# Kernel optimization log

Hardware: AMD Instinct MI355X
Metric: run time of the kernel (lower is better)

Reference implementation:

```python
import jax, jax.numpy as jnp
import numpy as np

B, H, E = 16384, 2048, 64
BASE_CF, MIN_CF, MAX_CF = 1.25, 1.0, 2.0


def setup_inputs() -> dict:
    key = jax.random.key(0)
    ks = jax.random.split(key, 4)
    return {
        "hidden_states": jax.random.normal(ks[0], (B, H), jnp.float32),
        "router_w": (jax.random.normal(ks[1], (E, H), jnp.float32) * 0.02),
        "cap_w1": (jax.random.normal(ks[2], (H // 4, H), jnp.float32) * 0.02),
        "cap_b1": jnp.zeros((H // 4,), jnp.float32),
        "cap_w2": (jax.random.normal(ks[3], (E, H // 4), jnp.float32) * 0.02),
        "cap_b2": jnp.zeros((E,), jnp.float32),
    }


def reference(hidden_states, router_w, cap_w1, cap_b1, cap_w2, cap_b2):
    n_tok = hidden_states.shape[0]
    n_exp = router_w.shape[0]

    # router
    router_logits = hidden_states @ router_w.T                      # [B, E]
    router_probs = jax.nn.softmax(router_logits, axis=-1)           # [B, E]

    # dynamic capacity prediction from mean token
    mean_h = hidden_states.mean(axis=0)                             # [H]
    h = jax.nn.relu(mean_h @ cap_w1.T + cap_b1)                     # [H/4]
    cap_logits = h @ cap_w2.T + cap_b2                              # [E]
    cap_weights = jax.nn.softmax(cap_logits)
    cap_factors = jnp.clip(BASE_CF + (cap_weights - 0.5) * (MAX_CF - MIN_CF), MIN_CF, MAX_CF)
    # int() truncation in torch == floor for positive values
    capacity = jnp.floor(n_tok * cap_factors / n_exp).astype(jnp.int32)  # [E]

    # per-expert descending rank of each token's prob (double argsort)
    ranks = jnp.argsort(jnp.argsort(-router_probs, axis=0), axis=0)      # [B, E]
    in_topk = ranks < capacity[None, :]                                  # [B, E]

    e_idx = jnp.arange(n_exp, dtype=jnp.int32)
    sel = jnp.max(jnp.where(in_topk, e_idx[None, :], -1), axis=1)        # [B]
    selections = jnp.where(sel >= 0, sel, 0).astype(jnp.int32)
    w = jnp.take_along_axis(router_probs, selections[:, None], axis=1)[:, 0]
    weights = jnp.where(sel >= 0, w, 0.0)

    entropy = -(router_probs * jnp.log(router_probs + 1e-8)).sum(axis=-1).mean()
    return router_logits, selections[:, None], weights[:, None], entropy
```

## Files before the change

### kernel.cpp

```cpp
#include <hip/hip_runtime.h>
#include <cstdint>

#define TOK 16384
#define HD 2048
#define NE 64
#define HQ 512
#define KC 64
#define NCH (HD / KC)
#define ESCALE 1073741824.0f

__global__ __launch_bounds__(256, 2) void k_router(const float* __restrict__ hid,
                                                   const float* __restrict__ rw,
                                                   float* __restrict__ logits,
                                                   float* __restrict__ csP) {
  __shared__ __align__(16) float As[2][32][KC];
  __shared__ __align__(16) float Bs[2][64][KC];
  __shared__ float red[2][4][64];
  const int tid = threadIdx.x;
  const int lane = tid & 63;
  const int w = tid >> 6;
  const int tm = lane >> 3, tn = lane & 7;
  const int tsub = w >> 1, ehalf = w & 1;
  const int t0 = blockIdx.x * 32;
  const int arow = tid >> 3;
  const int apr = tid & 7;
  const int brow = tid >> 2;
  const int bpr = (tid & 3) * 2;
  const float* hap = hid + (size_t)(t0 + arow) * HD + apr * 8;
  const float* bap = rw + (size_t)brow * HD + (tid & 3) * 16;
  const int aswz = arow & 7;
  const int bswz = (brow >> 2) & 7;
  const int aoff = ((apr ^ aswz) << 3);
  const int boff0 = (((bpr + 0) ^ bswz) << 3);
  const int boff1 = (((bpr + 1) ^ bswz) << 3);

  float4 va0 = *(const float4*)(hap);
  float4 va1 = *(const float4*)(hap + 4);
  float4 vb0 = *(const float4*)(bap);
  float4 vb1 = *(const float4*)(bap + 4);
  float4 vb2 = *(const float4*)(bap + 8);
  float4 vb3 = *(const float4*)(bap + 12);

  float acc[2][4];
#pragma unroll
  for (int i = 0; i < 2; ++i)
#pragma unroll
    for (int j = 0; j < 4; ++j) acc[i][j] = 0.f;

  const int rA0 = tsub * 16 + tm;
  const int rB0 = ehalf * 32 + tn * 4;

  for (int c = 0; c < NCH; ++c) {
    const int cur = c & 1;
    *(float4*)&As[cur][arow][aoff] = va0;
    *(float4*)&As[cur][arow][aoff + 4] = va1;
    *(float4*)&Bs[cur][brow][boff0] = vb0;
    *(float4*)&Bs[cur][brow][boff0 + 4] = vb1;
    *(float4*)&Bs[cur][brow][boff1] = vb2;
    *(float4*)&Bs[cur][brow][boff1 + 4] = vb3;
    if (c + 1 < NCH) {
      va0 = *(const float4*)(hap + (c + 1) * KC);
      va1 = *(const float4*)(hap + (c + 1) * KC + 4);
      vb0 = *(const float4*)(bap + (c + 1) * KC);
      vb1 = *(const float4*)(bap + (c + 1) * KC + 4);
      vb2 = *(const float4*)(bap + (c + 1) * KC + 8);
      vb3 = *(const float4*)(bap + (c + 1) * KC + 12);
    }
    __syncthreads();
    if (c > 0 && tid < 64) {
      const int pb = cur ^ 1;
      float v = red[pb][0][tid] + red[pb][1][tid] + red[pb][2][tid] + red[pb][3][tid];
      csP[(size_t)blockIdx.x * HD + (c - 1) * KC + tid] = v;
    }
    {
      const int col = tid & 63, grp = tid >> 6;
      float s = 0.f;
#pragma unroll
      for (int i = 0; i < 8; ++i) {
        const int row = grp * 8 + i;
        s += As[cur][row][(((col >> 3) ^ (row & 7)) << 3) + (col & 7)];
      }
      red[cur][grp][col] = s;
    }
#pragma unroll
    for (int qp = 0; qp < 8; ++qp) {
      const int oa = ((qp ^ tm) << 3);
      const int ob = ((qp ^ tn) << 3);
#pragma unroll
      for (int h = 0; h < 2; ++h) {
        float4 a0 = *(const float4*)&As[cur][rA0][oa + h * 4];
        float4 a1 = *(const float4*)&As[cur][rA0 + 8][oa + h * 4];
        float4 b0 = *(const float4*)&Bs[cur][rB0 + 0][ob + h * 4];
        float4 b1 = *(const float4*)&Bs[cur][rB0 + 1][ob + h * 4];
        float4 b2 = *(const float4*)&Bs[cur][rB0 + 2][ob + h * 4];
        float4 b3 = *(const float4*)&Bs[cur][rB0 + 3][ob + h * 4];
        acc[0][0] = fmaf(a0.x, b0.x, acc[0][0]);
        acc[0][0] = fmaf(a0.y, b0.y, acc[0][0]);
        acc[0][0] = fmaf(a0.z, b0.z, acc[0][0]);
        acc[0][0] = fmaf(a0.w, b0.w, acc[0][0]);
        acc[0][1] = fmaf(a0.x, b1.x, acc[0][1]);
        acc[0][1] = fmaf(a0.y, b1.y, acc[0][1]);
        acc[0][1] = fmaf(a0.z, b1.z, acc[0][1]);
        acc[0][1] = fmaf(a0.w, b1.w, acc[0][1]);
        acc[0][2] = fmaf(a0.x, b2.x, acc[0][2]);
        acc[0][2] = fmaf(a0.y, b2.y, acc[0][2]);
        acc[0][2] = fmaf(a0.z, b2.z, acc[0][2]);
        acc[0][2] = fmaf(a0.w, b2.w, acc[0][2]);
        acc[0][3] = fmaf(a0.x, b3.x, acc[0][3]);
        acc[0][3] = fmaf(a0.y, b3.y, acc[0][3]);
        acc[0][3] = fmaf(a0.z, b3.z, acc[0][3]);
        acc[0][3] = fmaf(a0.w, b3.w, acc[0][3]);
        acc[1][0] = fmaf(a1.x, b0.x, acc[1][0]);
        acc[1][0] = fmaf(a1.y, b0.y, acc[1][0]);
        acc[1][0] = fmaf(a1.z, b0.z, acc[1][0]);
        acc[1][0] = fmaf(a1.w, b0.w, acc[1][0]);
        acc[1][1] = fmaf(a1.x, b1.x, acc[1][1]);
        acc[1][1] = fmaf(a1.y, b1.y, acc[1][1]);
        acc[1][1] = fmaf(a1.z, b1.z, acc[1][1]);
        acc[1][1] = fmaf(a1.w, b1.w, acc[1][1]);
        acc[1][2] = fmaf(a1.x, b2.x, acc[1][2]);
        acc[1][2] = fmaf(a1.y, b2.y, acc[1][2]);
        acc[1][2] = fmaf(a1.z, b2.z, acc[1][2]);
        acc[1][2] = fmaf(a1.w, b2.w, acc[1][2]);
        acc[1][3] = fmaf(a1.x, b3.x, acc[1][3]);
        acc[1][3] = fmaf(a1.y, b3.y, acc[1][3]);
        acc[1][3] = fmaf(a1.z, b3.z, acc[1][3]);
        acc[1][3] = fmaf(a1.w, b3.w, acc[1][3]);
      }
    }
  }
  __syncthreads();
  if (tid < 64) {
    float v = red[1][0][tid] + red[1][1][tid] + red[1][2][tid] + red[1][3][tid];
    csP[(size_t)blockIdx.x * HD + (NCH - 1) * KC + tid] = v;
  }
  const int tA = t0 + tsub * 16 + tm;
  const int eA = ehalf * 32 + tn * 4;
  *(float4*)&logits[(size_t)tA * NE + eA] = make_float4(acc[0][0], acc[0][1], acc[0][2], acc[0][3]);
  *(float4*)&logits[(size_t)(tA + 8) * NE + eA] = make_float4(acc[1][0], acc[1][1], acc[1][2], acc[1][3]);
}

__global__ __launch_bounds__(256) void k_reduce_cs(const float* __restrict__ csP,
                                                   float* __restrict__ colsum) {
  __shared__ float rr[4][64];
  const int tid = threadIdx.x;
  const int k = blockIdx.x * 64 + (tid & 63);
  const int part = tid >> 6;
  float s = 0.f;
  for (int b = part * 128; b < part * 128 + 128; ++b)
    s += csP[(size_t)b * HD + k];
  rr[part][tid & 63] = s;
  __syncthreads();
  if (tid < 64)
    colsum[blockIdx.x * 64 + tid] = rr[0][tid] + rr[1][tid] + rr[2][tid] + rr[3][tid];
}

__global__ __launch_bounds__(256) void k_cap1(const float* __restrict__ w1,
                                              const float* __restrict__ b1,
                                              const float* __restrict__ colsum,
                                              float* __restrict__ h) {
  const int row = blockIdx.x;
  const int tid = threadIdx.x;
  const float invB = 1.0f / 16384.0f;
  const float* wr = w1 + (size_t)row * HD;
  float4 a0 = *(const float4*)(wr + tid * 4);
  float4 a1 = *(const float4*)(wr + 1024 + tid * 4);
  float4 c0 = *(const float4*)(colsum + tid * 4);
  float4 c1 = *(const float4*)(colsum + 1024 + tid * 4);
  float s = a0.x * (c0.x * invB) + a0.y * (c0.y * invB) +
            a0.z * (c0.z * invB) + a0.w * (c0.w * invB) +
            a1.x * (c1.x * invB) + a1.y * (c1.y * invB) +
            a1.z * (c1.z * invB) + a1.w * (c1.w * invB);
#pragma unroll
  for (int off = 32; off; off >>= 1) s += __shfl_down(s, off);
  __shared__ float wsum[4];
  if ((tid & 63) == 0) wsum[tid >> 6] = s;
  __syncthreads();
  if (tid == 0) {
    float t = wsum[0] + wsum[1] + wsum[2] + wsum[3] + b1[row];
    h[row] = fmaxf(t, 0.f);
  }
}

__global__ __launch_bounds__(128) void k_cap2(const float* __restrict__ w2,
                                              const float* __restrict__ b2,
                                              const float* __restrict__ h,
                                              float* __restrict__ cl) {
  const int e = blockIdx.x, tid = threadIdx.x;
  float4 a = *(const float4*)(w2 + (size_t)e * HQ + tid * 4);
  float4 hv = *(const float4*)(h + tid * 4);
  float s = a.x * hv.x + a.y * hv.y + a.z * hv.z + a.w * hv.w;
#pragma unroll
  for (int off = 32; off; off >>= 1) s += __shfl_down(s, off);
  __shared__ float wsum[2];
  if ((tid & 63) == 0) wsum[tid >> 6] = s;
  __syncthreads();
  if (tid == 0) cl[e] = wsum[0] + wsum[1] + b2[e];
}

__global__ __launch_bounds__(64) void k_capacity(const float* __restrict__ cl,
                                                 int* __restrict__ cap) {
  const int tid = threadIdx.x;
  float l = cl[tid];
  float m = l;
#pragma unroll
  for (int off = 1; off < 64; off <<= 1) m = fmaxf(m, __shfl_xor(m, off));
  float ex = expf(l - m);
  float s = ex;
#pragma unroll
  for (int off = 1; off < 64; off <<= 1) s += __shfl_xor(s, off);
  float w = ex / s;
  float cf = 1.25f + (w - 0.5f) * 1.0f;
  cf = fminf(fmaxf(cf, 1.0f), 2.0f);
  cap[tid] = (int)floorf(16384.0f * cf / 64.0f);
}

__global__ __launch_bounds__(256) void k_softmax(const float* __restrict__ logits,
                                                 float* __restrict__ probsT,
                                                 unsigned long long* __restrict__ ent) {
  __shared__ float tpT[64][65];
  __shared__ float sw[4];
  const int tid = threadIdx.x;
  const int lane = tid & 63;
  const int wv = tid >> 6;
  const int t0 = blockIdx.x * 64;
  const int tt = tid >> 2, q = tid & 3;
  const float* lr = logits + (size_t)(t0 + tt) * NE + q * 16;
  float4 v0 = *(const float4*)(lr);
  float4 v1 = *(const float4*)(lr + 4);
  float4 v2 = *(const float4*)(lr + 8);
  float4 v3 = *(const float4*)(lr + 12);
  float p[16] = {v0.x, v0.y, v0.z, v0.w, v1.x, v1.y, v1.z, v1.w,
                 v2.x, v2.y, v2.z, v2.w, v3.x, v3.y, v3.z, v3.w};
  float m = p[0];
#pragma unroll
  for (int i = 1; i < 16; ++i) m = fmaxf(m, p[i]);
  m = fmaxf(m, __shfl_xor(m, 1));
  m = fmaxf(m, __shfl_xor(m, 2));
  float s = 0.f;
#pragma unroll
  for (int i = 0; i < 16; ++i) { p[i] = expf(p[i] - m); s += p[i]; }
  s += __shfl_xor(s, 1);
  s += __shfl_xor(s, 2);
  const float inv = 1.0f / s;
  float el = 0.f;
#pragma unroll
  for (int i = 0; i < 16; ++i) {
    float pp = p[i] * inv;
    p[i] = pp;
    el += pp * logf(pp + 1e-8f);
  }
  el += __shfl_xor(el, 1);
  el += __shfl_xor(el, 2);
#pragma unroll
  for (int i = 0; i < 16; ++i) tpT[q * 16 + i][tt] = p[i];
  float ew = (q == 0) ? el : 0.f;
#pragma unroll
  for (int off = 4; off < 64; off <<= 1) ew += __shfl_xor(ew, off);
  if (lane == 0) sw[wv] = ew;
  __syncthreads();
  if (tid == 0) {
    float bt = sw[0] + sw[1] + sw[2] + sw[3];
    atomicAdd(ent, (unsigned long long)(long long)__float2ll_rn(bt * ESCALE));
  }
  const int er = tid >> 6, tl = tid & 63;
#pragma unroll
  for (int pass = 0; pass < 16; ++pass) {
    const int e = pass * 4 + er;
    probsT[(size_t)e * TOK + t0 + tl] = tpT[e][tl];
  }
}

__global__ __launch_bounds__(256) void k_selthr(const float* __restrict__ probsT,
                                                const int* __restrict__ cap,
                                                unsigned* __restrict__ thrT,
                                                int* __restrict__ cutoff) {
  const int e = blockIdx.x, tid = threadIdx.x;
  const uint4* col4 = (const uint4*)(probsT + (size_t)e * TOK);
  const unsigned* col = (const unsigned*)(probsT + (size_t)e * TOK);
  __shared__ unsigned hist[2048];
  __shared__ int wsfx[256];
  __shared__ unsigned sh_pref;
  __shared__ int sh_rem;
  __shared__ int sred[4], sgt[4], seq2[4];
  const int k = cap[e];
  unsigned prefix = 0, pmask = 0;
  int rem = k;
#pragma unroll
  for (int pass = 0; pass < 3; ++pass) {
    const int shift = (pass == 0) ? 21 : (pass == 1) ? 10 : 0;
    const int nb = (pass == 2) ? 1024 : 2048;
    const unsigned bmask = nb - 1;
    for (int i = tid; i < nb; i += 256) hist[i] = 0;
    __syncthreads();
    for (int it = 0; it < TOK / 1024; ++it) {
      uint4 v = col4[it * 256 + tid];
      if ((v.x & pmask) == prefix) atomicAdd(&hist[(v.x >> shift) & bmask], 1u);
      if ((v.y & pmask) == prefix) atomicAdd(&hist[(v.y >> shift) & bmask], 1u);
      if ((v.z & pmask) == prefix) atomicAdd(&hist[(v.z >> shift) & bmask], 1u);
      if ((v.w & pmask) == prefix) atomicAdd(&hist[(v.w >> shift) & bmask], 1u);
    }
    __syncthreads();
    const int cs = nb >> 8;
    const int base = tid * cs;
    int s = 0;
    for (int m2 = 0; m2 < cs; ++m2) s += (int)hist[base + m2];
    wsfx[tid] = s;
    __syncthreads();
    for (int off = 1; off < 256; off <<= 1) {
      int v = (tid + off < 256) ? wsfx[tid + off] : 0;
      __syncthreads();
      wsfx[tid] += v;
      __syncthreads();
    }
    int r = (tid < 255) ? wsfx[tid + 1] : 0;
    for (int m2 = cs - 1; m2 >= 0; --m2) {
      int rb = r + (int)hist[base + m2];
      if (rb >= rem && r < rem) {
        sh_pref = prefix | ((unsigned)(base + m2) << shift);
        sh_rem = rem - r;
      }
      r = rb;
    }
    __syncthreads();
    prefix = sh_pref;
    rem = sh_rem;
    pmask |= bmask << shift;
    __syncthreads();
  }
  const unsigned T = prefix;
  int lgt = 0, leq = 0;
  for (int it = 0; it < TOK / 1024; ++it) {
    uint4 v = col4[it * 256 + tid];
    lgt += (v.x > T) + (v.y > T) + (v.z > T) + (v.w > T);
    leq += (v.x == T) + (v.y == T) + (v.z == T) + (v.w == T);
  }
#pragma unroll
  for (int off = 32; off; off >>= 1) {
    lgt += __shfl_down(lgt, off);
    leq += __shfl_down(leq, off);
  }
  if ((tid & 63) == 0) { sgt[tid >> 6] = lgt; seq2[tid >> 6] = leq; }
  __syncthreads();
  const int c_gt = sgt[0] + sgt[1] + sgt[2] + sgt[3];
  const int c_eq = seq2[0] + seq2[1] + seq2[2] + seq2[3];
  const int n_allowed = k - c_gt;
  int cut;
  if (n_allowed <= 0) {
    cut = -1;
  } else if (c_eq <= n_allowed) {
    cut = 0x7fffffff;
  } else {
    int lo = 0, hi = TOK - 1;
    while (lo < hi) {
      const int mid = (lo + hi) >> 1;
      int c = 0;
      for (int i = tid; i <= mid; i += 256) c += (col[i] == T);
#pragma unroll
      for (int off = 32; off; off >>= 1) c += __shfl_down(c, off);
      __syncthreads();
      if ((tid & 63) == 0) sred[tid >> 6] = c;
      __syncthreads();
      const int cnt = sred[0] + sred[1] + sred[2] + sred[3];
      if (cnt >= n_allowed) hi = mid; else lo = mid + 1;
    }
    cut = lo;
  }
  if (tid == 0) { thrT[e] = T; cutoff[e] = cut; }
}

__global__ __launch_bounds__(256) void k_final(const float* __restrict__ probsT,
                                               const unsigned* __restrict__ thrT,
                                               const int* __restrict__ cutoff,
                                               const unsigned long long* __restrict__ ent,
                                               float* __restrict__ out_sel,
                                               float* __restrict__ out_w,
                                               float* __restrict__ out_ent) {
  __shared__ float tp[64][65];
  __shared__ unsigned sT[64];
  __shared__ int sC[64];
  const int tid = threadIdx.x;
  const int t0 = blockIdx.x * 64;
  if (tid < 64) { sT[tid] = thrT[tid]; sC[tid] = cutoff[tid]; }
  const int er = tid >> 6, tl2 = tid & 63;
#pragma unroll
  for (int pass = 0; pass < 16; ++pass) {
    const int e = pass * 4 + er;
    tp[e][tl2] = probsT[(size_t)e * TOK + t0 + tl2];
  }
  __syncthreads();
  const int tl = tid >> 2, q = tid & 3;
  const int t_abs = t0 + tl;
  int best = -1;
  float bw = 0.f;
  for (int i = 15; i >= 0; --i) {
    const int e = q * 16 + i;
    const float p = tp[e][tl];
    const unsigned v = __float_as_uint(p);
    const unsigned T = sT[e];
    if (v > T || (v == T && t_abs <= sC[e])) { best = e; bw = p; break; }
  }
#pragma unroll
  for (int off = 1; off <= 2; off <<= 1) {
    const int b2 = __shfl_xor(best, off);
    const float w2 = __shfl_xor(bw, off);
    if (b2 > best) { best = b2; bw = w2; }
  }
  if (q == 0) {
    out_sel[t_abs] = (float)(best >= 0 ? best : 0);
    out_w[t_abs] = (best >= 0 ? bw : 0.0f);
  }
  if (blockIdx.x == 0 && tid == 0)
    out_ent[0] = -((float)(long long)ent[0] * (1.0f / ESCALE)) / 16384.0f;
}

extern "C" void kernel_launch(void* const* d_in, const int* in_sizes, int n_in,
                              void* d_out, int out_size, void* d_ws, size_t ws_size,
                              hipStream_t stream) {
  (void)in_sizes; (void)n_in; (void)out_size; (void)ws_size;
  const float* hid = (const float*)d_in[0];
  const float* rw  = (const float*)d_in[1];
  const float* w1  = (const float*)d_in[2];
  const float* b1  = (const float*)d_in[3];
  const float* w2  = (const float*)d_in[4];
  const float* b2  = (const float*)d_in[5];
  float* out = (float*)d_out;
  float* logits  = out;
  float* out_sel = out + (size_t)TOK * NE;
  float* out_w   = out_sel + TOK;
  float* out_ent = out_w + TOK;
  char* ws = (char*)d_ws;
  float*              colsum = (float*)(ws + 0);
  unsigned long long* ent    = (unsigned long long*)(ws + 8192);
  float*              h      = (float*)(ws + 8448);
  float*              cl     = (float*)(ws + 10496);
  int*                cap    = (int*)(ws + 10752);
  unsigned*           thr    = (unsigned*)(ws + 11008);
  int*                cut    = (int*)(ws + 11264);
  float*              csP    = (float*)(ws + 16384);
  float*              probsT = (float*)(ws + 16384 + (size_t)512 * HD * 4);

  hipMemsetAsync(ent, 0, 8, stream);
  hipLaunchKernelGGL(k_router, dim3(TOK / 32), dim3(256), 0, stream, hid, rw, logits, csP);
  hipLaunchKernelGGL(k_reduce_cs, dim3(HD / 64), dim3(256), 0, stream, csP, colsum);
  hipLaunchKernelGGL(k_cap1, dim3(HQ), dim3(256), 0, stream, w1, b1, colsum, h);
  hipLaunchKernelGGL(k_cap2, dim3(NE), dim3(128), 0, stream, w2, b2, h, cl);
  hipLaunchKernelGGL(k_capacity, dim3(1), dim3(64), 0, stream, cl, cap);
  hipLaunchKernelGGL(k_softmax, dim3(TOK / 64), dim3(256), 0, stream, logits, probsT, ent);
  hipLaunchKernelGGL(k_selthr, dim3(NE), dim3(256), 0, stream, probsT, cap, thr, cut);
  hipLaunchKernelGGL(k_final, dim3(TOK / 64), dim3(256), 0, stream,
                     probsT, thr, cut, ent, out_sel, out_w, out_ent);
}
```

Baseline: 152.2 us.

## Split router GEMM over K, merge cap kernels, widen threshold-select blocks

The router GEMM now splits the hidden dimension into two halves, which doubles the grid and uses a smaller K chunk with higher occupancy (launch bounds 4). The second half's partial logits go to a scratch buffer, and the softmax kernel adds them back into the logits. The two small capacity-head kernels are merged into one launch, and the per-expert threshold selection uses 512-thread blocks. Together these aim to fill more CUs in the GEMM and cut launch overhead, at the cost of extra partial-sum traffic and buffers that now share workspace (probsT overlaps csP).

```diff
diff --git a/kernel.cpp b/kernel.cpp
--- a/kernel.cpp
+++ b/kernel.cpp
@@ -5,139 +5,138 @@
 #define HD 2048
 #define NE 64
 #define HQ 512
-#define KC 64
-#define NCH (HD / KC)
+#define KSPLIT 2
+#define KSL (HD / KSPLIT)
+#define KC 32
+#define NCH (KSL / KC)
 #define ESCALE 1073741824.0f
-
-__global__ __launch_bounds__(256, 2) void k_router(const float* __restrict__ hid,
+#define STB 512
+
+__global__ __launch_bounds__(256, 4) void k_router(const float* __restrict__ hid,
                                                    const float* __restrict__ rw,
                                                    float* __restrict__ logits,
+                                                   float* __restrict__ P1,
                                                    float* __restrict__ csP) {
   __shared__ __align__(16) float As[2][32][KC];
   __shared__ __align__(16) float Bs[2][64][KC];
-  __shared__ float red[2][4][64];
+  __shared__ float red[2][8][32];
   const int tid = threadIdx.x;
   const int lane = tid & 63;
   const int w = tid >> 6;
   const int tm = lane >> 3, tn = lane & 7;
   const int tsub = w >> 1, ehalf = w & 1;
-  const int t0 = blockIdx.x * 32;
+  const int bid = blockIdx.x;
+  const int tg = bid >> 1, ks = bid & 1;
+  const int t0 = tg * 32;
+  const int k0 = ks * KSL;
   const int arow = tid >> 3;
-  const int apr = tid & 7;
+  const int acol4 = tid & 7;
+  const int aoff = ((acol4 ^ (arow & 7)) << 2);
   const int brow = tid >> 2;
-  const int bpr = (tid & 3) * 2;
-  const float* hap = hid + (size_t)(t0 + arow) * HD + apr * 8;
-  const float* bap = rw + (size_t)brow * HD + (tid & 3) * 16;
-  const int aswz = arow & 7;
+  const int bc0 = (tid & 3) * 2;
   const int bswz = (brow >> 2) & 7;
-  const int aoff = ((apr ^ aswz) << 3);
-  const int boff0 = (((bpr + 0) ^ bswz) << 3);
-  const int boff1 = (((bpr + 1) ^ bswz) << 3);
-
-  float4 va0 = *(const float4*)(hap);
-  float4 va1 = *(const float4*)(hap + 4);
-  float4 vb0 = *(const float4*)(bap);
-  float4 vb1 = *(const float4*)(bap + 4);
-  float4 vb2 = *(const float4*)(bap + 8);
-  float4 vb3 = *(const float4*)(bap + 12);
-
+  const int boff0 = (((bc0 + 0) ^ bswz) << 2);
+  const int boff1 = (((bc0 + 1) ^ bswz) << 2);
+  const float* hap = hid + (size_t)(t0 + arow) * HD + k0 + acol4 * 4;
+  const float* bap = rw + (size_t)brow * HD + k0 + bc0 * 4;
+  float4 a4 = *(const float4*)(hap);
+  float4 b40 = *(const float4*)(bap);
+  float4 b41 = *(const float4*)(bap + 4);
   float acc[2][4];
 #pragma unroll
   for (int i = 0; i < 2; ++i)
 #pragma unroll
     for (int j = 0; j < 4; ++j) acc[i][j] = 0.f;
-
-  const int rA0 = tsub * 16 + tm;
-  const int rB0 = ehalf * 32 + tn * 4;
+  const int rA = tsub * 16 + tm;
+  const int rB = ehalf * 32 + tn * 4;
+  const int cshalf = (tid >> 5) & 1;
+  const int csgrp = (tid >> 6) * 2 + cshalf;
+  const int cscol = tid & 31;
 
   for (int c = 0; c < NCH; ++c) {
     const int cur = c & 1;
-    *(float4*)&As[cur][arow][aoff] = va0;
-    *(float4*)&As[cur][arow][aoff + 4] = va1;
-    *(float4*)&Bs[cur][brow][boff0] = vb0;
-    *(float4*)&Bs[cur][brow][boff0 + 4] = vb1;
-    *(float4*)&Bs[cur][brow][boff1] = vb2;
-    *(float4*)&Bs[cur][brow][boff1 + 4] = vb3;
+    *(float4*)&As[cur][arow][aoff] = a4;
+    *(float4*)&Bs[cur][brow][boff0] = b40;
+    *(float4*)&Bs[cur][brow][boff1] = b41;
     if (c + 1 < NCH) {
-      va0 = *(const float4*)(hap + (c + 1) * KC);
-      va1 = *(const float4*)(hap + (c + 1) * KC + 4);
-      vb0 = *(const float4*)(bap + (c + 1) * KC);
-      vb1 = *(const float4*)(bap + (c + 1) * KC + 4);
-      vb2 = *(const float4*)(bap + (c + 1) * KC + 8);
-      vb3 = *(const float4*)(bap + (c + 1) * KC + 12);
-    }
-    __syncthreads();
-    if (c > 0 && tid < 64) {
+      a4 = *(const float4*)(hap + (c + 1) * KC);
+      b40 = *(const float4*)(bap + (c + 1) * KC);
+      b41 = *(const float4*)(bap + (c + 1) * KC + 4);
+    }
+    __syncthreads();
+    if (c > 0 && tid < 32) {
       const int pb = cur ^ 1;
-      float v = red[pb][0][tid] + red[pb][1][tid] + red[pb][2][tid] + red[pb][3][tid];
-      csP[(size_t)blockIdx.x * HD + (c - 1) * KC + tid] = v;
+      float v = red[pb][0][tid] + red[pb][1][tid] + red[pb][2][tid] +
+                red[pb][3][tid] + red[pb][4][tid] + red[pb][5][tid] +
+                red[pb][6][tid] + red[pb][7][tid];
+      csP[(size_t)bid * KSL + (c - 1) * KC + tid] = v;
     }
     {
-      const int col = tid & 63, grp = tid >> 6;
       float s = 0.f;
 #pragma unroll
-      for (int i = 0; i < 8; ++i) {
-        const int row = grp * 8 + i;
-        s += As[cur][row][(((col >> 3) ^ (row & 7)) << 3) + (col & 7)];
+      for (int i = 0; i < 4; ++i) {
+        const int row = csgrp * 4 + i;
+        s += As[cur][row][(((cscol >> 2) ^ (row & 7)) << 2) + (cscol & 3)];
       }
-      red[cur][grp][col] = s;
-    }
-#pragma unroll
-    for (int qp = 0; qp < 8; ++qp) {
-      const int oa = ((qp ^ tm) << 3);
-      const int ob = ((qp ^ tn) << 3);
-#pragma unroll
-      for (int h = 0; h < 2; ++h) {
-        float4 a0 = *(const float4*)&As[cur][rA0][oa + h * 4];
-        float4 a1 = *(const float4*)&As[cur][rA0 + 8][oa + h * 4];
-        float4 b0 = *(const float4*)&Bs[cur][rB0 + 0][ob + h * 4];
-        float4 b1 = *(const float4*)&Bs[cur][rB0 + 1][ob + h * 4];
-        float4 b2 = *(const float4*)&Bs[cur][rB0 + 2][ob + h * 4];
-        float4 b3 = *(const float4*)&Bs[cur][rB0 + 3][ob + h * 4];
-        acc[0][0] = fmaf(a0.x, b0.x, acc[0][0]);
-        acc[0][0] = fmaf(a0.y, b0.y, acc[0][0]);
-        acc[0][0] = fmaf(a0.z, b0.z, acc[0][0]);
-        acc[0][0] = fmaf(a0.w, b0.w, acc[0][0]);
-        acc[0][1] = fmaf(a0.x, b1.x, acc[0][1]);
-        acc[0][1] = fmaf(a0.y, b1.y, acc[0][1]);
-        acc[0][1] = fmaf(a0.z, b1.z, acc[0][1]);
-        acc[0][1] = fmaf(a0.w, b1.w, acc[0][1]);
-        acc[0][2] = fmaf(a0.x, b2.x, acc[0][2]);
-        acc[0][2] = fmaf(a0.y, b2.y, acc[0][2]);
-        acc[0][2] = fmaf(a0.z, b2.z, acc[0][2]);
-        acc[0][2] = fmaf(a0.w, b2.w, acc[0][2]);
-        acc[0][3] = fmaf(a0.x, b3.x, acc[0][3]);
-        acc[0][3] = fmaf(a0.y, b3.y, acc[0][3]);
-        acc[0][3] = fmaf(a0.z, b3.z, acc[0][3]);
-        acc[0][3] = fmaf(a0.w, b3.w, acc[0][3]);
-        acc[1][0] = fmaf(a1.x, b0.x, acc[1][0]);
-        acc[1][0] = fmaf(a1.y, b0.y, acc[1][0]);
-        acc[1][0] = fmaf(a1.z, b0.z, acc[1][0]);
-        acc[1][0] = fmaf(a1.w, b0.w, acc[1][0]);
-        acc[1][1] = fmaf(a1.x, b1.x, acc[1][1]);
-        acc[1][1] = fmaf(a1.y, b1.y, acc[1][1]);
-        acc[1][1] = fmaf(a1.z, b1.z, acc[1][1]);
-        acc[1][1] = fmaf(a1.w, b1.w, acc[1][1]);
-        acc[1][2] = fmaf(a1.x, b2.x, acc[1][2]);
-        acc[1][2] = fmaf(a1.y, b2.y, acc[1][2]);
-        acc[1][2] = fmaf(a1.z, b2.z, acc[1][2]);
-        acc[1][2] = fmaf(a1.w, b2.w, acc[1][2]);
-        acc[1][3] = fmaf(a1.x, b3.x, acc[1][3]);
-        acc[1][3] = fmaf(a1.y, b3.y, acc[1][3]);
-        acc[1][3] = fmaf(a1.z, b3.z, acc[1][3]);
-        acc[1][3] = fmaf(a1.w, b3.w, acc[1][3]);
-      }
-    }
-  }
-  __syncthreads();
-  if (tid < 64) {
-    float v = red[1][0][tid] + red[1][1][tid] + red[1][2][tid] + red[1][3][tid];
-    csP[(size_t)blockIdx.x * HD + (NCH - 1) * KC + tid] = v;
-  }
-  const int tA = t0 + tsub * 16 + tm;
-  const int eA = ehalf * 32 + tn * 4;
-  *(float4*)&logits[(size_t)tA * NE + eA] = make_float4(acc[0][0], acc[0][1], acc[0][2], acc[0][3]);
-  *(float4*)&logits[(size_t)(tA + 8) * NE + eA] = make_float4(acc[1][0], acc[1][1], acc[1][2], acc[1][3]);
+      red[cur][csgrp][cscol] = s;
+    }
+#pragma unroll
+    for (int q = 0; q < 8; ++q) {
+      const int oa = (q ^ tm) << 2;
+      const int ob = (q ^ tn) << 2;
+      float4 a0 = *(const float4*)&As[cur][rA][oa];
+      float4 a1 = *(const float4*)&As[cur][rA + 8][oa];
+      float4 b0 = *(const float4*)&Bs[cur][rB + 0][ob];
+      float4 b1 = *(const float4*)&Bs[cur][rB + 1][ob];
+      float4 b2 = *(const float4*)&Bs[cur][rB + 2][ob];
+      float4 b3 = *(const float4*)&Bs[cur][rB + 3][ob];
+      acc[0][0] = fmaf(a0.x, b0.x, acc[0][0]);
+      acc[0][0] = fmaf(a0.y, b0.y, acc[0][0]);
+      acc[0][0] = fmaf(a0.z, b0.z, acc[0][0]);
+      acc[0][0] = fmaf(a0.w, b0.w, acc[0][0]);
+      acc[0][1] = fmaf(a0.x, b1.x, acc[0][1]);
+      acc[0][1] = fmaf(a0.y, b1.y, acc[0][1]);
+      acc[0][1] = fmaf(a0.z, b1.z, acc[0][1]);
+      acc[0][1] = fmaf(a0.w, b1.w, acc[0][1]);
+      acc[0][2] = fmaf(a0.x, b2.x, acc[0][2]);
+      acc[0][2] = fmaf(a0.y, b2.y, acc[0][2]);
+      acc[0][2] = fmaf(a0.z, b2.z, acc[0][2]);
+      acc[0][2] = fmaf(a0.w, b2.w, acc[0][2]);
+      acc[0][3] = fmaf(a0.x, b3.x, acc[0][3]);
+      acc[0][3] = fmaf(a0.y, b3.y, acc[0][3]);
+      acc[0][3] = fmaf(a0.z, b3.z, acc[0][3]);
+      acc[0][3] = fmaf(a0.w, b3.w, acc[0][3]);
+      acc[1][0] = fmaf(a1.x, b0.x, acc[1][0]);
+      acc[1][0] = fmaf(a1.y, b0.y, acc[1][0]);
+      acc[1][0] = fmaf(a1.z, b0.z, acc[1][0]);
+      acc[1][0] = fmaf(a1.w, b0.w, acc[1][0]);
+      acc[1][1] = fmaf(a1.x, b1.x, acc[1][1]);
+      acc[1][1] = fmaf(a1.y, b1.y, acc[1][1]);
+      acc[1][1] = fmaf(a1.z, b1.z, acc[1][1]);
+      acc[1][1] = fmaf(a1.w, b1.w, acc[1][1]);
+      acc[1][2] = fmaf(a1.x, b2.x, acc[1][2]);
+      acc[1][2] = fmaf(a1.y, b2.y, acc[1][2]);
+      acc[1][2] = fmaf(a1.z, b2.z, acc[1][2]);
+      acc[1][2] = fmaf(a1.w, b2.w, acc[1][2]);
+      acc[1][3] = fmaf(a1.x, b3.x, acc[1][3]);
+      acc[1][3] = fmaf(a1.y, b3.y, acc[1][3]);
+      acc[1][3] = fmaf(a1.z, b3.z, acc[1][3]);
+      acc[1][3] = fmaf(a1.w, b3.w, acc[1][3]);
+    }
+  }
+  __syncthreads();
+  if (tid < 32) {
+    float v = red[1][0][tid] + red[1][1][tid] + red[1][2][tid] +
+              red[1][3][tid] + red[1][4][tid] + red[1][5][tid] +
+              red[1][6][tid] + red[1][7][tid];
+    csP[(size_t)bid * KSL + (NCH - 1) * KC + tid] = v;
+  }
+  float* outp = (ks == 0) ? logits : P1;
+  const int tA = t0 + rA;
+  *(float4*)&outp[(size_t)tA * NE + rB] =
+      make_float4(acc[0][0], acc[0][1], acc[0][2], acc[0][3]);
+  *(float4*)&outp[(size_t)(tA + 8) * NE + rB] =
+      make_float4(acc[1][0], acc[1][1], acc[1][2], acc[1][3]);
 }
 
 __global__ __launch_bounds__(256) void k_reduce_cs(const float* __restrict__ csP,
@@ -145,10 +144,11 @@
   __shared__ float rr[4][64];
   const int tid = threadIdx.x;
   const int k = blockIdx.x * 64 + (tid & 63);
+  const int ks = k >> 10, ko = k & 1023;
   const int part = tid >> 6;
   float s = 0.f;
-  for (int b = part * 128; b < part * 128 + 128; ++b)
-    s += csP[(size_t)b * HD + k];
+  for (int tg = part * 128; tg < part * 128 + 128; ++tg)
+    s += csP[(size_t)(tg * 2 + ks) * KSL + ko];
   rr[part][tid & 63] = s;
   __syncthreads();
   if (tid < 64)
@@ -182,40 +182,44 @@
   }
 }
 
-__global__ __launch_bounds__(128) void k_cap2(const float* __restrict__ w2,
-                                              const float* __restrict__ b2,
-                                              const float* __restrict__ h,
-                                              float* __restrict__ cl) {
-  const int e = blockIdx.x, tid = threadIdx.x;
-  float4 a = *(const float4*)(w2 + (size_t)e * HQ + tid * 4);
-  float4 hv = *(const float4*)(h + tid * 4);
-  float s = a.x * hv.x + a.y * hv.y + a.z * hv.z + a.w * hv.w;
-#pragma unroll
-  for (int off = 32; off; off >>= 1) s += __shfl_down(s, off);
-  __shared__ float wsum[2];
-  if ((tid & 63) == 0) wsum[tid >> 6] = s;
-  __syncthreads();
-  if (tid == 0) cl[e] = wsum[0] + wsum[1] + b2[e];
-}
-
-__global__ __launch_bounds__(64) void k_capacity(const float* __restrict__ cl,
+__global__ __launch_bounds__(256) void k_caphead(const float* __restrict__ w2,
+                                                 const float* __restrict__ b2,
+                                                 const float* __restrict__ h,
                                                  int* __restrict__ cap) {
-  const int tid = threadIdx.x;
-  float l = cl[tid];
-  float m = l;
-#pragma unroll
-  for (int off = 1; off < 64; off <<= 1) m = fmaxf(m, __shfl_xor(m, off));
-  float ex = expf(l - m);
-  float s = ex;
-#pragma unroll
-  for (int off = 1; off < 64; off <<= 1) s += __shfl_xor(s, off);
-  float w = ex / s;
-  float cf = 1.25f + (w - 0.5f) * 1.0f;
-  cf = fminf(fmaxf(cf, 1.0f), 2.0f);
-  cap[tid] = (int)floorf(16384.0f * cf / 64.0f);
-}
-
-__global__ __launch_bounds__(256) void k_softmax(const float* __restrict__ logits,
+  __shared__ float clS[64];
+  const int tid = threadIdx.x;
+  const int e = tid >> 2, part = tid & 3;
+  const float* wr = w2 + (size_t)e * HQ + part * 128;
+  const float* hp = h + part * 128;
+  float s = 0.f;
+#pragma unroll
+  for (int i = 0; i < 32; ++i) {
+    float4 a = *(const float4*)(wr + i * 4);
+    float4 hv = *(const float4*)(hp + i * 4);
+    s += a.x * hv.x + a.y * hv.y + a.z * hv.z + a.w * hv.w;
+  }
+  s += __shfl_down(s, 1);
+  s += __shfl_down(s, 2);
+  if (part == 0) clS[e] = s + b2[e];
+  __syncthreads();
+  if (tid < 64) {
+    float l = clS[tid];
+    float m = l;
+#pragma unroll
+    for (int off = 1; off < 64; off <<= 1) m = fmaxf(m, __shfl_xor(m, off));
+    float ex = expf(l - m);
+    float sum = ex;
+#pragma unroll
+    for (int off = 1; off < 64; off <<= 1) sum += __shfl_xor(sum, off);
+    float wgt = ex / sum;
+    float cf = 1.25f + (wgt - 0.5f) * 1.0f;
+    cf = fminf(fmaxf(cf, 1.0f), 2.0f);
+    cap[tid] = (int)floorf(16384.0f * cf / 64.0f);
+  }
+}
+
+__global__ __launch_bounds__(256) void k_softmax(float* __restrict__ logits,
+                                                 const float* __restrict__ P1,
                                                  float* __restrict__ probsT,
                                                  unsigned long long* __restrict__ ent) {
   __shared__ float tpT[64][65];
@@ -225,21 +229,28 @@
   const int wv = tid >> 6;
   const int t0 = blockIdx.x * 64;
   const int tt = tid >> 2, q = tid & 3;
-  const float* lr = logits + (size_t)(t0 + tt) * NE + q * 16;
-  float4 v0 = *(const float4*)(lr);
-  float4 v1 = *(const float4*)(lr + 4);
-  float4 v2 = *(const float4*)(lr + 8);
-  float4 v3 = *(const float4*)(lr + 12);
-  float p[16] = {v0.x, v0.y, v0.z, v0.w, v1.x, v1.y, v1.z, v1.w,
-                 v2.x, v2.y, v2.z, v2.w, v3.x, v3.y, v3.z, v3.w};
-  float m = p[0];
-#pragma unroll
-  for (int i = 1; i < 16; ++i) m = fmaxf(m, p[i]);
+  float* lr = logits + (size_t)(t0 + tt) * NE + q * 16;
+  const float* pr = P1 + (size_t)(t0 + tt) * NE + q * 16;
+  float l[16];
+#pragma unroll
+  for (int i = 0; i < 16; i += 4) {
+    float4 v0 = *(const float4*)(lr + i);
+    float4 v1 = *(const float4*)(pr + i);
+    l[i + 0] = v0.x + v1.x; l[i + 1] = v0.y + v1.y;
+    l[i + 2] = v0.z + v1.z; l[i + 3] = v0.w + v1.w;
+  }
+#pragma unroll
+  for (int i = 0; i < 16; i += 4)
+    *(float4*)(lr + i) = make_float4(l[i], l[i + 1], l[i + 2], l[i + 3]);
+  float m = l[0];
+#pragma unroll
+  for (int i = 1; i < 16; ++i) m = fmaxf(m, l[i]);
   m = fmaxf(m, __shfl_xor(m, 1));
   m = fmaxf(m, __shfl_xor(m, 2));
+  float p[16];
   float s = 0.f;
 #pragma unroll
-  for (int i = 0; i < 16; ++i) { p[i] = expf(p[i] - m); s += p[i]; }
+  for (int i = 0; i < 16; ++i) { p[i] = expf(l[i] - m); s += p[i]; }
   s += __shfl_xor(s, 1);
   s += __shfl_xor(s, 2);
   const float inv = 1.0f / s;
@@ -271,7 +282,7 @@
   }
 }
 
-__global__ __launch_bounds__(256) void k_selthr(const float* __restrict__ probsT,
+__global__ __launch_bounds__(STB) void k_selthr(const float* __restrict__ probsT,
                                                 const int* __restrict__ cap,
                                                 unsigned* __restrict__ thrT,
                                                 int* __restrict__ cutoff) {
@@ -279,10 +290,10 @@
   const uint4* col4 = (const uint4*)(probsT + (size_t)e * TOK);
   const unsigned* col = (const unsigned*)(probsT + (size_t)e * TOK);
   __shared__ unsigned hist[2048];
-  __shared__ int wsfx[256];
+  __shared__ int wsfx[STB];
   __shared__ unsigned sh_pref;
   __shared__ int sh_rem;
-  __shared__ int sred[4], sgt[4], seq2[4];
+  __shared__ int sred[8], sgt[8], seq2[8];
   const int k = cap[e];
   unsigned prefix = 0, pmask = 0;
   int rem = k;
@@ -291,29 +302,29 @@
     const int shift = (pass == 0) ? 21 : (pass == 1) ? 10 : 0;
     const int nb = (pass == 2) ? 1024 : 2048;
     const unsigned bmask = nb - 1;
-    for (int i = tid; i < nb; i += 256) hist[i] = 0;
-    __syncthreads();
-    for (int it = 0; it < TOK / 1024; ++it) {
-      uint4 v = col4[it * 256 + tid];
+    for (int i = tid; i < nb; i += STB) hist[i] = 0;
+    __syncthreads();
+    for (int it = 0; it < TOK / (4 * STB); ++it) {
+      uint4 v = col4[it * STB + tid];
       if ((v.x & pmask) == prefix) atomicAdd(&hist[(v.x >> shift) & bmask], 1u);
       if ((v.y & pmask) == prefix) atomicAdd(&hist[(v.y >> shift) & bmask], 1u);
       if ((v.z & pmask) == prefix) atomicAdd(&hist[(v.z >> shift) & bmask], 1u);
       if ((v.w & pmask) == prefix) atomicAdd(&hist[(v.w >> shift) & bmask], 1u);
     }
     __syncthreads();
-    const int cs = nb >> 8;
+    const int cs = nb / STB;
     const int base = tid * cs;
     int s = 0;
     for (int m2 = 0; m2 < cs; ++m2) s += (int)hist[base + m2];
     wsfx[tid] = s;
     __syncthreads();
-    for (int off = 1; off < 256; off <<= 1) {
-      int v = (tid + off < 256) ? wsfx[tid + off] : 0;
+    for (int off = 1; off < STB; off <<= 1) {
+      int v = (tid + off < STB) ? wsfx[tid + off] : 0;
       __syncthreads();
       wsfx[tid] += v;
       __syncthreads();
     }
-    int r = (tid < 255) ? wsfx[tid + 1] : 0;
+    int r = (tid < STB - 1) ? wsfx[tid + 1] : 0;
     for (int m2 = cs - 1; m2 >= 0; --m2) {
       int rb = r + (int)hist[base + m2];
       if (rb >= rem && r < rem) {
@@ -330,8 +341,8 @@
   }
   const unsigned T = prefix;
   int lgt = 0, leq = 0;
-  for (int it = 0; it < TOK / 1024; ++it) {
-    uint4 v = col4[it * 256 + tid];
+  for (int it = 0; it < TOK / (4 * STB); ++it) {
+    uint4 v = col4[it * STB + tid];
     lgt += (v.x > T) + (v.y > T) + (v.z > T) + (v.w > T);
     leq += (v.x == T) + (v.y == T) + (v.z == T) + (v.w == T);
   }
@@ -342,8 +353,9 @@
   }
   if ((tid & 63) == 0) { sgt[tid >> 6] = lgt; seq2[tid >> 6] = leq; }
   __syncthreads();
-  const int c_gt = sgt[0] + sgt[1] + sgt[2] + sgt[3];
-  const int c_eq = seq2[0] + seq2[1] + seq2[2] + seq2[3];
+  int c_gt = 0, c_eq = 0;
+#pragma unroll
+  for (int i = 0; i < 8; ++i) { c_gt += sgt[i]; c_eq += seq2[i]; }
   const int n_allowed = k - c_gt;
   int cut;
   if (n_allowed <= 0) {
@@ -355,13 +367,15 @@
     while (lo < hi) {
       const int mid = (lo + hi) >> 1;
       int c = 0;
-      for (int i = tid; i <= mid; i += 256) c += (col[i] == T);
+      for (int i = tid; i <= mid; i += STB) c += (col[i] == T);
 #pragma unroll
       for (int off = 32; off; off >>= 1) c += __shfl_down(c, off);
       __syncthreads();
       if ((tid & 63) == 0) sred[tid >> 6] = c;
       __syncthreads();
-      const int cnt = sred[0] + sred[1] + sred[2] + sred[3];
+      int cnt = 0;
+#pragma unroll
+      for (int i = 0; i < 8; ++i) cnt += sred[i];
       if (cnt >= n_allowed) hi = mid; else lo = mid + 1;
     }
     cut = lo;
@@ -433,21 +447,22 @@
   float*              colsum = (float*)(ws + 0);
   unsigned long long* ent    = (unsigned long long*)(ws + 8192);
   float*              h      = (float*)(ws + 8448);
-  float*              cl     = (float*)(ws + 10496);
   int*                cap    = (int*)(ws + 10752);
   unsigned*           thr    = (unsigned*)(ws + 11008);
   int*                cut    = (int*)(ws + 11264);
   float*              csP    = (float*)(ws + 16384);
-  float*              probsT = (float*)(ws + 16384 + (size_t)512 * HD * 4);
+  float*              probsT = (float*)(ws + 16384);
+  float*              P1     = (float*)(ws + 16384 + (size_t)1024 * KSL * 4);
 
   hipMemsetAsync(ent, 0, 8, stream);
-  hipLaunchKernelGGL(k_router, dim3(TOK / 32), dim3(256), 0, stream, hid, rw, logits, csP);
+  hipLaunchKernelGGL(k_router, dim3(TOK / 32 * KSPLIT), dim3(256), 0, stream,
+                     hid, rw, logits, P1, csP);
   hipLaunchKernelGGL(k_reduce_cs, dim3(HD / 64), dim3(256), 0, stream, csP, colsum);
   hipLaunchKernelGGL(k_cap1, dim3(HQ), dim3(256), 0, stream, w1, b1, colsum, h);
-  hipLaunchKernelGGL(k_cap2, dim3(NE), dim3(128), 0, stream, w2, b2, h, cl);
-  hipLaunchKernelGGL(k_capacity, dim3(1), dim3(64), 0, stream, cl, cap);
-  hipLaunchKernelGGL(k_softmax, dim3(TOK / 64), dim3(256), 0, stream, logits, probsT, ent);
-  hipLaunchKernelGGL(k_selthr, dim3(NE), dim3(256), 0, stream, probsT, cap, thr, cut);
+  hipLaunchKernelGGL(k_caphead, dim3(1), dim3(256), 0, stream, w2, b2, h, cap);
+  hipLaunchKernelGGL(k_softmax, dim3(TOK / 64), dim3(256), 0, stream,
+                     logits, P1, probsT, ent);
+  hipLaunchKernelGGL(k_selthr, dim3(NE), dim3(STB), 0, stream, probsT, cap, thr, cut);
   hipLaunchKernelGGL(k_final, dim3(TOK / 64), dim3(256), 0, stream,
                      probsT, thr, cut, ent, out_sel, out_w, out_ent);
 }
```

Measured after the change: 201.2 us. 1.32x slower.
